# Kernel tuning notes

Measured on AMD Instinct MI355X. Metric: run time of the kernel, lower is better.

Reference implementation:

```python
import jax, jax.numpy as jnp
import numpy as np

B, T, H = 32, 64, 1024  # batch_size, input_number, hidden_size


def _lstm_cell(x, h, c, Wih, Whh, bih, bhh):
    # torch.nn.LSTMCell math: gate order i, f, g, o
    gates = x @ Wih.T + bih + h @ Whh.T + bhh
    i, f, g, o = jnp.split(gates, 4, axis=-1)
    c = jax.nn.sigmoid(f) * c + jax.nn.sigmoid(i) * jnp.tanh(g)
    h = jax.nn.sigmoid(o) * jnp.tanh(c)
    return h, c


def setup_inputs() -> dict:
    key = jax.random.key(0)
    ks = iter(jax.random.split(key, 64))

    def unif(shape, fan):
        s = 1.0 / np.sqrt(fan)
        return jax.random.uniform(next(ks), shape, jnp.float32, -s, s)

    inp = {
        'apperances': jax.random.normal(next(ks), (B, T, 2 * H), jnp.float32),
        'motions': jax.random.normal(next(ks), (B, T, 2 * H), jnp.float32),
    }
    # four LSTM cells: 1a/1m take 2H input, 2a/2m take H input
    for name, in_dim in [('1a', 2 * H), ('2a', H), ('1m', 2 * H), ('2m', H)]:
        inp['Wih_' + name] = unif((4 * H, in_dim), H)
        inp['Whh_' + name] = unif((4 * H, H), H)
        inp['bih_' + name] = unif((4 * H,), H)
        inp['bhh_' + name] = unif((4 * H,), H)
    # two-stream memory fusion (stand-in for MemoryRamTwoStreamModule)
    inp['Wg'] = unif((H, 2 * H), 2 * H)
    inp['bg'] = unif((H,), 2 * H)
    inp['Wa'] = unif((H, H), H)
    inp['ba'] = unif((H,), H)
    inp['Wm'] = unif((H, H), H)
    inp['bm'] = unif((H,), H)
    return inp


def reference(apperances, motions,
              Wih_1a, Whh_1a, bih_1a, bhh_1a,
              Wih_2a, Whh_2a, bih_2a, bhh_2a,
              Wih_1m, Whh_1m, bih_1m, bhh_1m,
              Wih_2m, Whh_2m, bih_2m, bhh_2m,
              Wg, bg, Wa, ba, Wm, bm):
    b, t, _ = apperances.shape
    h = Whh_1a.shape[1]
    xa = jnp.swapaxes(apperances, 0, 1)  # (T, B, 2H)
    xm = jnp.swapaxes(motions, 0, 1)     # (T, B, 2H)
    z = jnp.zeros((b, h), apperances.dtype)

    def step(carry, xs):
        h1a, c1a, h2a, c2a, h1m, c1m, h2m, c2m = carry
        xa_t, xm_t = xs
        h1m, c1m = _lstm_cell(xm_t, h1m, c1m, Wih_1m, Whh_1m, bih_1m, bhh_1m)
        h2m, c2m = _lstm_cell(h1m, h2m, c2m, Wih_2m, Whh_2m, bih_2m, bhh_2m)
        h1a, c1a = _lstm_cell(xa_t, h1a, c1a, Wih_1a, Whh_1a, bih_1a, bhh_1a)
        h2a, c2a = _lstm_cell(h1a, h2a, c2a, Wih_2a, Whh_2a, bih_2a, bhh_2a)
        return (h1a, c1a, h2a, c2a, h1m, c1m, h2m, c2m), (h2a, h2m)

    _, (Ha, Hm) = jax.lax.scan(step, (z, z, z, z, z, z, z, z), (xa, xm))
    Ha = jnp.swapaxes(Ha, 0, 1)  # (B, T, H)
    Hm = jnp.swapaxes(Hm, 0, 1)  # (B, T, H)
    # gated two-stream fusion per timestep (assumed MemoryRamTwoStreamModule)
    g = jax.nn.sigmoid(jnp.einsum('btk,hk->bth', jnp.concatenate([Ha, Hm], -1), Wg) + bg)
    mem = g * jnp.tanh(Ha @ Wa.T + ba) + (1.0 - g) * jnp.tanh(Hm @ Wm.T + bm)
    return mem  # (B, T, H)
```

## Files before the change

kernel.cpp:

```cpp
#include <hip/hip_runtime.h>
#include <cstdint>

typedef _Float16 f16;
typedef _Float16 f16x4v __attribute__((ext_vector_type(4)));
typedef _Float16 f16x8 __attribute__((ext_vector_type(8)));
typedef float f32x4 __attribute__((ext_vector_type(4)));

#define DEV static __device__ __forceinline__

#define GLDS16(gp, lp) __builtin_amdgcn_global_load_lds( \
    (const __attribute__((address_space(1))) void*)(gp), \
    (__attribute__((address_space(3))) void*)(lp), 16, 0, 0)

DEV float sigf(float x) { return 1.0f / (1.0f + __expf(-x)); }
DEV float tanh2(float x) {
  float e = __expf(-2.0f * fabsf(x));
  float t = (1.0f - e) / (1.0f + e);
  return x >= 0.0f ? t : -t;
}

DEV void waitflags(const unsigned* fp, int l) {
  unsigned f;
  do {
    f = __hip_atomic_load(fp + l, __ATOMIC_RELAXED, __HIP_MEMORY_SCOPE_AGENT);
  } while (__any(f == 0));
  asm volatile("" ::: "memory");
  __builtin_amdgcn_sched_barrier(0);
}

__global__ __launch_bounds__(256) void k_cvt(const float* __restrict__ s,
                                             f16* __restrict__ d, int n) {
  int i = (blockIdx.x * 256 + threadIdx.x) * 4;
  if (i >= n) return;
  float4 v = *(const float4*)(s + i);
  f16x4v o;
  o.x = (f16)v.x; o.y = (f16)v.y; o.z = (f16)v.z; o.w = (f16)v.w;
  *(f16x4v*)(d + i) = o;
}

__global__ __launch_bounds__(256) void k_packw1(const float* __restrict__ W,
                                                f16* __restrict__ P) {
  int i2 = blockIdx.x * 256 + threadIdx.x;
  int l = i2 & 63, frag = i2 >> 6;
  int kt = frag & 31, ug = frag >> 5;
  int gate = ug & 3, ut = ug >> 2;
  int row = gate * 1024 + ut * 16 + (l & 15);
  int k = kt * 32 + 8 * (l >> 4);
  const float* s = W + row * 1024 + k;
  f16x8 o;
#pragma unroll
  for (int j = 0; j < 8; ++j) o[j] = (f16)s[j];
  *(f16x8*)(P + frag * 512 + l * 8) = o;
}

__global__ __launch_bounds__(256) void k_packw2(const float* __restrict__ Wih,
                                                const float* __restrict__ Whh,
                                                f16* __restrict__ P) {
  int i2 = blockIdx.x * 256 + threadIdx.x;
  int l = i2 & 63, frag = i2 >> 6;
  int kt = frag & 63, ug = frag >> 6;
  int gate = ug & 3, ut = ug >> 2;
  int row = gate * 1024 + ut * 16 + (l & 15);
  int k = kt * 32 + 8 * (l >> 4);
  const float* s = (k < 1024) ? (Wih + row * 1024 + k)
                              : (Whh + row * 1024 + (k - 1024));
  f16x8 o;
#pragma unroll
  for (int j = 0; j < 8; ++j) o[j] = (f16)s[j];
  *(f16x8*)(P + frag * 512 + l * 8) = o;
}

template <int NKT, int LDA>
__global__ __launch_bounds__(256) void k_igemm(
    const f16* __restrict__ A0, const f16* __restrict__ A1,
    const f16* __restrict__ B0, const f16* __restrict__ B1,
    const float* __restrict__ bi0, const float* __restrict__ bh0,
    const float* __restrict__ bi1, const float* __restrict__ bh1,
    f16* __restrict__ C0, f16* __restrict__ C1) {
  const f16* A = blockIdx.z ? A1 : A0;
  const f16* B = blockIdx.z ? B1 : B0;
  const float* bi = blockIdx.z ? bi1 : bi0;
  const float* bh = blockIdx.z ? bh1 : bh0;
  f16* C = blockIdx.z ? C1 : C0;

  __shared__ alignas(16) f16 As[128 * 64];
  __shared__ alignas(16) f16 Bs[128 * 64];

  int tid = threadIdx.x, l = tid & 63, w = tid >> 6;
  int m0 = blockIdx.x * 128, n0 = blockIdx.y * 128;
  int wm = (w & 1) * 64, wn = (w >> 1) * 64;
  int lr = l & 15, lg = l >> 4;
  int sr = w * 32 + (l >> 3);
  int sc = (l & 7) * 8;

  f32x4 acc[4][4];
  f32x4 zero = {0.f, 0.f, 0.f, 0.f};
#pragma unroll
  for (int mt = 0; mt < 4; ++mt)
#pragma unroll
    for (int nt = 0; nt < 4; ++nt) acc[mt][nt] = zero;

  for (int kt = 0; kt < NKT; ++kt) {
    int k0 = kt * 64;
#pragma unroll
    for (int c2 = 0; c2 < 4; ++c2) {
      GLDS16(A + (size_t)(m0 + sr + c2 * 8) * LDA + k0 + sc, &As[(w * 32 + c2 * 8) * 64]);
      GLDS16(B + (size_t)(n0 + sr + c2 * 8) * LDA + k0 + sc, &Bs[(w * 32 + c2 * 8) * 64]);
    }
    __syncthreads();
#pragma unroll
    for (int ks = 0; ks < 2; ++ks) {
      f16x8 af[4], bf[4];
#pragma unroll
      for (int mt = 0; mt < 4; ++mt)
        af[mt] = *(const f16x8*)&As[(wm + mt * 16 + lr) * 64 + ks * 32 + 8 * lg];
#pragma unroll
      for (int nt = 0; nt < 4; ++nt)
        bf[nt] = *(const f16x8*)&Bs[(wn + nt * 16 + lr) * 64 + ks * 32 + 8 * lg];
#pragma unroll
      for (int mt = 0; mt < 4; ++mt)
#pragma unroll
        for (int nt = 0; nt < 4; ++nt)
          acc[mt][nt] = __builtin_amdgcn_mfma_f32_16x16x32_f16(af[mt], bf[nt], acc[mt][nt], 0, 0, 0);
    }
    __syncthreads();
  }

#pragma unroll
  for (int nt = 0; nt < 4; ++nt) {
    int n = n0 + wn + nt * 16 + lr;
    float bsum = bi[n] + bh[n];
#pragma unroll
    for (int mt = 0; mt < 4; ++mt) {
      int m = m0 + wm + mt * 16 + lg * 4;
#pragma unroll
      for (int r = 0; r < 4; ++r)
        C[(size_t)(m + r) * 4096 + n] = (f16)(acc[mt][nt][r] + bsum);
    }
  }
}

__global__ __launch_bounds__(512, 1) void k_scan2(
    const f16* __restrict__ Wp1_a, const f16* __restrict__ Wp1_m,
    const f16* __restrict__ Wp2_a, const f16* __restrict__ Wp2_m,
    const f16* __restrict__ G_a, const f16* __restrict__ G_m,
    const float* __restrict__ bi2_a, const float* __restrict__ bh2_a,
    const float* __restrict__ bi2_m, const float* __restrict__ bh2_m,
    f16* __restrict__ H1h,
    f16* __restrict__ h2c,
    f16* __restrict__ HaHm,
    unsigned* __restrict__ flags1,
    unsigned* __restrict__ flags2) {
  int bi = blockIdx.x;
  int role = bi >> 7, s = (bi >> 6) & 1, ut = bi & 63, u0 = ut * 16;
  int tid = threadIdx.x, l = tid & 63, w = tid >> 6;
  int lr = l & 15, lg = l >> 4;
  const f16* G = s ? G_m : G_a;
  f16* H1s = H1h + (size_t)s * 64 * 32768;
  f16* h2s = h2c + (size_t)s * 64 * 32768;
  f16* H2o = HaHm + s * 1024;

  f16x8 wreg[8][4];
  if (role == 0) {
    const f16* Wp = s ? Wp1_m : Wp1_a;
#pragma unroll
    for (int ks = 0; ks < 4; ++ks)
#pragma unroll
      for (int g = 0; g < 4; ++g) {
        wreg[ks][g] = *(const f16x8*)(Wp + (size_t)((ut * 4 + g) * 32 + (w * 4 + ks)) * 512 + l * 8);
        asm volatile("" : "+v"(wreg[ks][g]));
      }
  } else {
    const f16* Wp = s ? Wp2_m : Wp2_a;
#pragma unroll
    for (int ks = 0; ks < 8; ++ks)
#pragma unroll
      for (int g = 0; g < 4; ++g) {
        wreg[ks][g] = *(const f16x8*)(Wp + (size_t)((ut * 4 + g) * 64 + (w * 8 + ks)) * 512 + l * 8);
        asm volatile("" : "+v"(wreg[ks][g]));
      }
  }

  __shared__ alignas(16) float red[8][64][33];
  __shared__ alignas(16) f16 Gs[32][4][16];

  int eb = tid >> 4, eu = tid & 15;
  int emt = eb >> 4, elg = (eb >> 2) & 3, er = eb & 3;
  int lred = elg * 16 + eu;
  int idxb = emt * 16 + er;
  float creg = 0.f;
  f32x4 zero = {0.f, 0.f, 0.f, 0.f};

  if (role == 0) {
    int pb = tid >> 4, pg2 = (tid >> 2) & 3, p4 = tid & 3;
    int cb = w * 128;
    for (int t = 0; t < 64; ++t) {
      f16x4v gfrag = *(const f16x4v*)(G + (size_t)(pb * 64 + t) * 4096 + pg2 * 1024 + u0 + p4 * 4);

      f32x4 acc[2][4];
#pragma unroll
      for (int mt = 0; mt < 2; ++mt)
#pragma unroll
        for (int g = 0; g < 4; ++g) acc[mt][g] = zero;

      if (t > 0) {
        if (w == 0) waitflags(flags1 + (size_t)(s * 64 + t - 1) * 64, l);
        __syncthreads();
        const f16* hp = H1s + (size_t)(t - 1) * 32768;
        f16x8 A0[4], A1[4];
#pragma unroll
        for (int ks = 0; ks < 4; ++ks) {
          int col = cb + ks * 32 + 8 * lg;
          A0[ks] = *(const f16x8*)(hp + lr * 1024 + col);
          A1[ks] = *(const f16x8*)(hp + (16 + lr) * 1024 + col);
        }
#pragma unroll
        for (int ks = 0; ks < 4; ++ks)
#pragma unroll
          for (int g = 0; g < 4; ++g) {
            acc[0][g] = __builtin_amdgcn_mfma_f32_16x16x32_f16(A0[ks], wreg[ks][g], acc[0][g], 0, 0, 0);
            acc[1][g] = __builtin_amdgcn_mfma_f32_16x16x32_f16(A1[ks], wreg[ks][g], acc[1][g], 0, 0, 0);
          }
      }

      *(f16x4v*)&Gs[pb][pg2][p4 * 4] = gfrag;
#pragma unroll
      for (int mt = 0; mt < 2; ++mt)
#pragma unroll
        for (int g = 0; g < 4; ++g)
#pragma unroll
          for (int r = 0; r < 4; ++r)
            red[w][l][(mt * 4 + g) * 4 + r] = acc[mt][g][r];
      __syncthreads();

      float pre[4];
#pragma unroll
      for (int g = 0; g < 4; ++g) {
        int idx = idxb + g * 4;
        pre[g] = red[0][lred][idx] + red[1][lred][idx] + red[2][lred][idx] +
                 red[3][lred][idx] + red[4][lred][idx] + red[5][lred][idx] +
                 red[6][lred][idx] + red[7][lred][idx] + (float)Gs[eb][g][eu];
      }
      float cn = sigf(pre[1]) * creg + sigf(pre[0]) * tanh2(pre[2]);
      creg = cn;
      union { unsigned short us; f16 h; } cv;
      cv.h = (f16)(sigf(pre[3]) * tanh2(cn));
      unsigned ov = (unsigned)__shfl_xor((int)(unsigned)cv.us, 1, 64);
      if (!(tid & 1)) {
        unsigned pkv = ((unsigned)cv.us) | (ov << 16);
        __hip_atomic_store((unsigned*)(H1s + (size_t)t * 32768 + eb * 1024 + u0 + eu), pkv,
                           __ATOMIC_RELAXED, __HIP_MEMORY_SCOPE_AGENT);
      }
      asm volatile("s_waitcnt vmcnt(0)" ::: "memory");
      __syncthreads();
      if (tid == 0)
        __hip_atomic_store(flags1 + (size_t)(s * 64 + t) * 64 + ut, 1u,
                           __ATOMIC_RELAXED, __HIP_MEMORY_SCOPE_AGENT);
    }
  } else {
    const float* bip = s ? bi2_m : bi2_a;
    const float* bhp = s ? bh2_m : bh2_a;
    float b2r[4];
#pragma unroll
    for (int g = 0; g < 4; ++g)
      b2r[g] = bip[g * 1024 + u0 + eu] + bhp[g * 1024 + u0 + eu];
    int cb = (w & 3) * 256;

    for (int t = 0; t < 64; ++t) {
      f32x4 acc[2][4];
#pragma unroll
      for (int mt = 0; mt < 2; ++mt)
#pragma unroll
        for (int g = 0; g < 4; ++g) acc[mt][g] = zero;

      if (w == 0) waitflags(flags1 + (size_t)(s * 64 + t) * 64, l);
      if (t > 0 && w == 4) waitflags(flags2 + (size_t)(s * 64 + t - 1) * 64, l);
      __syncthreads();

      if (w < 4) {
        const f16* hp = H1s + (size_t)t * 32768;
        f16x8 A0[4], A1[4], B0[4], B1[4];
#pragma unroll
        for (int ks = 0; ks < 4; ++ks) {
          int c0 = cb + ks * 32 + 8 * lg;
          int c1 = cb + (4 + ks) * 32 + 8 * lg;
          A0[ks] = *(const f16x8*)(hp + lr * 1024 + c0);
          A1[ks] = *(const f16x8*)(hp + (16 + lr) * 1024 + c0);
          B0[ks] = *(const f16x8*)(hp + lr * 1024 + c1);
          B1[ks] = *(const f16x8*)(hp + (16 + lr) * 1024 + c1);
        }
#pragma unroll
        for (int ks = 0; ks < 4; ++ks)
#pragma unroll
          for (int g = 0; g < 4; ++g) {
            acc[0][g] = __builtin_amdgcn_mfma_f32_16x16x32_f16(A0[ks], wreg[ks][g], acc[0][g], 0, 0, 0);
            acc[1][g] = __builtin_amdgcn_mfma_f32_16x16x32_f16(A1[ks], wreg[ks][g], acc[1][g], 0, 0, 0);
          }
#pragma unroll
        for (int ks = 0; ks < 4; ++ks)
#pragma unroll
          for (int g = 0; g < 4; ++g) {
            acc[0][g] = __builtin_amdgcn_mfma_f32_16x16x32_f16(B0[ks], wreg[4 + ks][g], acc[0][g], 0, 0, 0);
            acc[1][g] = __builtin_amdgcn_mfma_f32_16x16x32_f16(B1[ks], wreg[4 + ks][g], acc[1][g], 0, 0, 0);
          }
      } else if (t > 0) {
        const f16* hp = h2s + (size_t)(t - 1) * 32768;
        f16x8 A0[4], A1[4], B0[4], B1[4];
#pragma unroll
        for (int ks = 0; ks < 4; ++ks) {
          int c0 = cb + ks * 32 + 8 * lg;
          int c1 = cb + (4 + ks) * 32 + 8 * lg;
          A0[ks] = *(const f16x8*)(hp + lr * 1024 + c0);
          A1[ks] = *(const f16x8*)(hp + (16 + lr) * 1024 + c0);
          B0[ks] = *(const f16x8*)(hp + lr * 1024 + c1);
          B1[ks] = *(const f16x8*)(hp + (16 + lr) * 1024 + c1);
        }
#pragma unroll
        for (int ks = 0; ks < 4; ++ks)
#pragma unroll
          for (int g = 0; g < 4; ++g) {
            acc[0][g] = __builtin_amdgcn_mfma_f32_16x16x32_f16(A0[ks], wreg[ks][g], acc[0][g], 0, 0, 0);
            acc[1][g] = __builtin_amdgcn_mfma_f32_16x16x32_f16(A1[ks], wreg[ks][g], acc[1][g], 0, 0, 0);
          }
#pragma unroll
        for (int ks = 0; ks < 4; ++ks)
#pragma unroll
          for (int g = 0; g < 4; ++g) {
            acc[0][g] = __builtin_amdgcn_mfma_f32_16x16x32_f16(B0[ks], wreg[4 + ks][g], acc[0][g], 0, 0, 0);
            acc[1][g] = __builtin_amdgcn_mfma_f32_16x16x32_f16(B1[ks], wreg[4 + ks][g], acc[1][g], 0, 0, 0);
          }
      }

#pragma unroll
      for (int mt = 0; mt < 2; ++mt)
#pragma unroll
        for (int g = 0; g < 4; ++g)
#pragma unroll
          for (int r = 0; r < 4; ++r)
            red[w][l][(mt * 4 + g) * 4 + r] = acc[mt][g][r];
      __syncthreads();

      float pre[4];
#pragma unroll
      for (int g = 0; g < 4; ++g) {
        int idx = idxb + g * 4;
        pre[g] = red[0][lred][idx] + red[1][lred][idx] + red[2][lred][idx] +
                 red[3][lred][idx] + red[4][lred][idx] + red[5][lred][idx] +
                 red[6][lred][idx] + red[7][lred][idx] + b2r[g];
      }
      float cn = sigf(pre[1]) * creg + sigf(pre[0]) * tanh2(pre[2]);
      creg = cn;
      union { unsigned short us; f16 h; } cv;
      cv.h = (f16)(sigf(pre[3]) * tanh2(cn));
      unsigned ov = (unsigned)__shfl_xor((int)(unsigned)cv.us, 1, 64);
      if (!(tid & 1)) {
        unsigned pkv = ((unsigned)cv.us) | (ov << 16);
        __hip_atomic_store((unsigned*)(h2s + (size_t)t * 32768 + eb * 1024 + u0 + eu), pkv,
                           __ATOMIC_RELAXED, __HIP_MEMORY_SCOPE_AGENT);
        *(unsigned*)(H2o + (size_t)(eb * 64 + t) * 2048 + u0 + eu) = pkv;
      }
      asm volatile("s_waitcnt vmcnt(0)" ::: "memory");
      __syncthreads();
      if (tid == 0)
        __hip_atomic_store(flags2 + (size_t)(s * 64 + t) * 64 + ut, 1u,
                           __ATOMIC_RELAXED, __HIP_MEMORY_SCOPE_AGENT);
    }
  }
}

DEV void gemm_phase(const f16* __restrict__ H, int kA0,
                    const f16* __restrict__ Bp, int brs, int nk,
                    f16* As, f16* Bs, int m0, int n0, int w, int l,
                    int wm, int wn, f32x4 (&acc)[4][2]) {
  f32x4 zero = {0.f, 0.f, 0.f, 0.f};
#pragma unroll
  for (int mt = 0; mt < 4; ++mt)
#pragma unroll
    for (int nt = 0; nt < 2; ++nt) acc[mt][nt] = zero;
  int lr = l & 15, lg = l >> 4;
  int sc = (l & 7) * 8;
  for (int kt = 0; kt < nk; ++kt) {
    int ka = kA0 + kt * 64, kb = kt * 64;
#pragma unroll
    for (int c2 = 0; c2 < 4; ++c2)
      GLDS16(H + (size_t)(m0 + w * 32 + c2 * 8 + (l >> 3)) * 2048 + ka + sc,
             As + (w * 32 + c2 * 8) * 64);
#pragma unroll
    for (int c2 = 0; c2 < 2; ++c2)
      GLDS16(Bp + (size_t)(n0 + w * 16 + c2 * 8 + (l >> 3)) * brs + kb + sc,
             Bs + (w * 16 + c2 * 8) * 64);
    __syncthreads();
#pragma unroll
    for (int ks = 0; ks < 2; ++ks) {
      f16x8 af[4], bf[2];
#pragma unroll
      for (int mt = 0; mt < 4; ++mt)
        af[mt] = *(const f16x8*)&As[(wm + mt * 16 + lr) * 64 + ks * 32 + 8 * lg];
#pragma unroll
      for (int nt = 0; nt < 2; ++nt)
        bf[nt] = *(const f16x8*)&Bs[(wn + nt * 16 + lr) * 64 + ks * 32 + 8 * lg];
#pragma unroll
      for (int mt = 0; mt < 4; ++mt)
#pragma unroll
        for (int nt = 0; nt < 2; ++nt)
          acc[mt][nt] = __builtin_amdgcn_mfma_f32_16x16x32_f16(af[mt], bf[nt], acc[mt][nt], 0, 0, 0);
    }
    __syncthreads();
  }
}

__global__ __launch_bounds__(256) void k_fusion(
    const f16* __restrict__ H, const f16* __restrict__ Wg16,
    const f16* __restrict__ Wa16, const f16* __restrict__ Wm16,
    const float* __restrict__ bg, const float* __restrict__ ba,
    const float* __restrict__ bm, float* __restrict__ out) {
  __shared__ alignas(16) f16 As[128 * 64];
  __shared__ alignas(16) f16 Bs[64 * 64];
  int tid = threadIdx.x, l = tid & 63, w = tid >> 6;
  int m0 = blockIdx.x * 128, n0 = blockIdx.y * 64;
  int wm = (w & 1) * 64, wn = (w >> 1) * 32;
  int lr = l & 15, lg = l >> 4;

  f32x4 acc[4][2];
  float ta[4][2][4], tm[4][2][4];

  gemm_phase(H, 0, Wa16, 1024, 16, As, Bs, m0, n0, w, l, wm, wn, acc);
#pragma unroll
  for (int nt = 0; nt < 2; ++nt) {
    float bv = ba[n0 + wn + nt * 16 + lr];
#pragma unroll
    for (int mt = 0; mt < 4; ++mt)
#pragma unroll
      for (int r = 0; r < 4; ++r) ta[mt][nt][r] = tanh2(acc[mt][nt][r] + bv);
  }
  gemm_phase(H, 1024, Wm16, 1024, 16, As, Bs, m0, n0, w, l, wm, wn, acc);
#pragma unroll
  for (int nt = 0; nt < 2; ++nt) {
    float bv = bm[n0 + wn + nt * 16 + lr];
#pragma unroll
    for (int mt = 0; mt < 4; ++mt)
#pragma unroll
      for (int r = 0; r < 4; ++r) tm[mt][nt][r] = tanh2(acc[mt][nt][r] + bv);
  }
  gemm_phase(H, 0, Wg16, 2048, 32, As, Bs, m0, n0, w, l, wm, wn, acc);
#pragma unroll
  for (int nt = 0; nt < 2; ++nt) {
    int n = n0 + wn + nt * 16 + lr;
    float bv = bg[n];
#pragma unroll
    for (int mt = 0; mt < 4; ++mt) {
      int m = m0 + wm + mt * 16 + lg * 4;
#pragma unroll
      for (int r = 0; r < 4; ++r) {
        float g = sigf(acc[mt][nt][r] + bv);
        out[(size_t)(m + r) * 1024 + n] = tm[mt][nt][r] + g * (ta[mt][nt][r] - tm[mt][nt][r]);
      }
    }
  }
}

extern "C" void kernel_launch(void* const* d_in, const int* in_sizes, int n_in,
                              void* d_out, int out_size, void* d_ws, size_t ws_size,
                              hipStream_t stream) {
  const float* xa = (const float*)d_in[0];
  const float* xm = (const float*)d_in[1];
  const float* Wih_1a = (const float*)d_in[2];
  const float* Whh_1a = (const float*)d_in[3];
  const float* bih_1a = (const float*)d_in[4];
  const float* bhh_1a = (const float*)d_in[5];
  const float* Wih_2a = (const float*)d_in[6];
  const float* Whh_2a = (const float*)d_in[7];
  const float* bih_2a = (const float*)d_in[8];
  const float* bhh_2a = (const float*)d_in[9];
  const float* Wih_1m = (const float*)d_in[10];
  const float* Whh_1m = (const float*)d_in[11];
  const float* bih_1m = (const float*)d_in[12];
  const float* bhh_1m = (const float*)d_in[13];
  const float* Wih_2m = (const float*)d_in[14];
  const float* Whh_2m = (const float*)d_in[15];
  const float* bih_2m = (const float*)d_in[16];
  const float* bhh_2m = (const float*)d_in[17];
  const float* Wg = (const float*)d_in[18];
  const float* bg = (const float*)d_in[19];
  const float* Wa = (const float*)d_in[20];
  const float* ba = (const float*)d_in[21];
  const float* Wm = (const float*)d_in[22];
  const float* bm = (const float*)d_in[23];

  char* ws = (char*)d_ws;
  const size_t MB = 1024ull * 1024;
  if (ws_size < 138 * MB) return;

  f16* x16a    = (f16*)(ws + 0 * MB);
  f16* x16m    = (f16*)(ws + 8 * MB);
  f16* W1ih16a = (f16*)(ws + 16 * MB);
  f16* W1ih16m = (f16*)(ws + 32 * MB);
  f16* W1p_a   = (f16*)(ws + 48 * MB);
  f16* W1p_m   = (f16*)(ws + 56 * MB);
  f16* W2p_a   = (f16*)(ws + 64 * MB);
  f16* W2p_m   = (f16*)(ws + 80 * MB);
  f16* Wg16    = (f16*)(ws + 96 * MB);
  f16* Wa16    = (f16*)(ws + 100 * MB);
  f16* Wm16    = (f16*)(ws + 102 * MB);
  f16* G0a     = (f16*)(ws + 104 * MB);
  f16* G0m     = (f16*)(ws + 120 * MB);
  unsigned* flags1 = (unsigned*)(ws + 136 * MB);
  unsigned* flags2 = (unsigned*)(ws + 136 * MB + 32768);
  f16* HaHm    = (f16*)(ws + 0 * MB);
  f16* H1h     = (f16*)(ws + 8 * MB);
  f16* h2c     = (f16*)(ws + 16 * MB);

  dim3 B256(256);
  k_cvt<<<4096, B256, 0, stream>>>(xa, x16a, 4194304);
  k_cvt<<<4096, B256, 0, stream>>>(xm, x16m, 4194304);
  k_cvt<<<8192, B256, 0, stream>>>(Wih_1a, W1ih16a, 8388608);
  k_cvt<<<8192, B256, 0, stream>>>(Wih_1m, W1ih16m, 8388608);
  k_cvt<<<2048, B256, 0, stream>>>(Wg, Wg16, 2097152);
  k_cvt<<<1024, B256, 0, stream>>>(Wa, Wa16, 1048576);
  k_cvt<<<1024, B256, 0, stream>>>(Wm, Wm16, 1048576);
  k_packw1<<<2048, B256, 0, stream>>>(Whh_1a, W1p_a);
  k_packw1<<<2048, B256, 0, stream>>>(Whh_1m, W1p_m);
  k_packw2<<<4096, B256, 0, stream>>>(Wih_2a, Whh_2a, W2p_a);
  k_packw2<<<4096, B256, 0, stream>>>(Wih_2m, Whh_2m, W2p_m);
  hipMemsetAsync(flags1, 0, 65536, stream);

  k_igemm<32, 2048><<<dim3(16, 32, 2), B256, 0, stream>>>(
      x16a, x16m, W1ih16a, W1ih16m, bih_1a, bhh_1a, bih_1m, bhh_1m, G0a, G0m);

  k_scan2<<<256, dim3(512), 0, stream>>>(
      W1p_a, W1p_m, W2p_a, W2p_m, G0a, G0m,
      bih_2a, bhh_2a, bih_2m, bhh_2m, H1h, h2c, HaHm, flags1, flags2);

  k_fusion<<<dim3(16, 16), B256, 0, stream>>>(HaHm, Wg16, Wa16, Wm16, bg, ba,
                                              bm, (float*)d_out);
}
```

Measured before the change: 755.4 us.

## Replace block barriers in scan with per-wave flag polling and LDS double buffering

The recurrent scan kernel stops using block-wide barriers around flag waits. Each wave now polls only the producer flags for the slice of H it reads, and publishes its step through a shared-memory counter so the last finishing wave sets the global flag. The reduction buffers are double-buffered by timestep parity so the trailing barrier can be removed, and the eleven preprocessing launches are merged into three kernels. This cuts barrier stalls and launch overhead on the latency-bound serial recurrence, but it adds twice the LDS for the reduction buffers and more intricate memory-ordering reasoning.

```diff
diff --git a/kernel.cpp b/kernel.cpp
--- a/kernel.cpp
+++ b/kernel.cpp
@@ -19,27 +19,36 @@
   return x >= 0.0f ? t : -t;
 }
 
-DEV void waitflags(const unsigned* fp, int l) {
-  unsigned f;
-  do {
-    f = __hip_atomic_load(fp + l, __ATOMIC_RELAXED, __HIP_MEMORY_SCOPE_AGENT);
-  } while (__any(f == 0));
-  asm volatile("" ::: "memory");
-  __builtin_amdgcn_sched_barrier(0);
-}
-
-__global__ __launch_bounds__(256) void k_cvt(const float* __restrict__ s,
-                                             f16* __restrict__ d, int n) {
-  int i = (blockIdx.x * 256 + threadIdx.x) * 4;
-  if (i >= n) return;
+__global__ __launch_bounds__(256) void k_cvt_all(
+    const float* __restrict__ s0, f16* __restrict__ d0,
+    const float* __restrict__ s1, f16* __restrict__ d1,
+    const float* __restrict__ s2, f16* __restrict__ d2,
+    const float* __restrict__ s3, f16* __restrict__ d3,
+    const float* __restrict__ s4, f16* __restrict__ d4,
+    const float* __restrict__ s5, f16* __restrict__ d5,
+    const float* __restrict__ s6, f16* __restrict__ d6) {
+  int bid = blockIdx.x;
+  const float* s; f16* d; int base;
+  if (bid < 4096)       { s = s0; d = d0; base = bid; }
+  else if (bid < 8192)  { s = s1; d = d1; base = bid - 4096; }
+  else if (bid < 16384) { s = s2; d = d2; base = bid - 8192; }
+  else if (bid < 24576) { s = s3; d = d3; base = bid - 16384; }
+  else if (bid < 26624) { s = s4; d = d4; base = bid - 24576; }
+  else if (bid < 27648) { s = s5; d = d5; base = bid - 26624; }
+  else                  { s = s6; d = d6; base = bid - 27648; }
+  int i = (base * 256 + threadIdx.x) * 4;
   float4 v = *(const float4*)(s + i);
   f16x4v o;
   o.x = (f16)v.x; o.y = (f16)v.y; o.z = (f16)v.z; o.w = (f16)v.w;
   *(f16x4v*)(d + i) = o;
 }
 
-__global__ __launch_bounds__(256) void k_packw1(const float* __restrict__ W,
-                                                f16* __restrict__ P) {
+__global__ __launch_bounds__(256) void k_packw1(const float* __restrict__ Wa,
+                                                const float* __restrict__ Wm,
+                                                f16* __restrict__ Pa,
+                                                f16* __restrict__ Pm) {
+  const float* W = blockIdx.y ? Wm : Wa;
+  f16* P = blockIdx.y ? Pm : Pa;
   int i2 = blockIdx.x * 256 + threadIdx.x;
   int l = i2 & 63, frag = i2 >> 6;
   int kt = frag & 31, ug = frag >> 5;
@@ -53,9 +62,15 @@
   *(f16x8*)(P + frag * 512 + l * 8) = o;
 }
 
-__global__ __launch_bounds__(256) void k_packw2(const float* __restrict__ Wih,
-                                                const float* __restrict__ Whh,
-                                                f16* __restrict__ P) {
+__global__ __launch_bounds__(256) void k_packw2(const float* __restrict__ Wiha,
+                                                const float* __restrict__ Whha,
+                                                const float* __restrict__ Wihm,
+                                                const float* __restrict__ Whhm,
+                                                f16* __restrict__ Pa,
+                                                f16* __restrict__ Pm) {
+  const float* Wih = blockIdx.y ? Wihm : Wiha;
+  const float* Whh = blockIdx.y ? Whhm : Whha;
+  f16* P = blockIdx.y ? Pm : Pa;
   int i2 = blockIdx.x * 256 + threadIdx.x;
   int l = i2 & 63, frag = i2 >> 6;
   int kt = frag & 63, ug = frag >> 6;
@@ -181,8 +196,11 @@
       }
   }
 
-  __shared__ alignas(16) float red[8][64][33];
-  __shared__ alignas(16) f16 Gs[32][4][16];
+  __shared__ alignas(16) float red[2][8][64][33];
+  __shared__ alignas(16) f16 Gs[2][32][4][16];
+  __shared__ unsigned wdone[64];
+  if (tid < 64) wdone[tid] = 0;
+  __syncthreads();
 
   int eb = tid >> 4, eu = tid & 15;
   int emt = eb >> 4, elg = (eb >> 2) & 3, er = eb & 3;
@@ -195,6 +213,7 @@
     int pb = tid >> 4, pg2 = (tid >> 2) & 3, p4 = tid & 3;
     int cb = w * 128;
     for (int t = 0; t < 64; ++t) {
+      int pp = t & 1;
       f16x4v gfrag = *(const f16x4v*)(G + (size_t)(pb * 64 + t) * 4096 + pg2 * 1024 + u0 + p4 * 4);
 
       f32x4 acc[2][4];
@@ -204,8 +223,14 @@
         for (int g = 0; g < 4; ++g) acc[mt][g] = zero;
 
       if (t > 0) {
-        if (w == 0) waitflags(flags1 + (size_t)(s * 64 + t - 1) * 64, l);
-        __syncthreads();
+        const unsigned* fp = flags1 + (size_t)(s * 64 + t - 1) * 64 + 8 * w;
+        unsigned f;
+        do {
+          f = (l < 8) ? __hip_atomic_load(fp + l, __ATOMIC_RELAXED,
+                                          __HIP_MEMORY_SCOPE_AGENT) : 1u;
+        } while (__any(f == 0));
+        asm volatile("" ::: "memory");
+        __builtin_amdgcn_sched_barrier(0);
         const f16* hp = H1s + (size_t)(t - 1) * 32768;
         f16x8 A0[4], A1[4];
 #pragma unroll
@@ -223,23 +248,25 @@
           }
       }
 
-      *(f16x4v*)&Gs[pb][pg2][p4 * 4] = gfrag;
+      *(f16x4v*)&Gs[pp][pb][pg2][p4 * 4] = gfrag;
 #pragma unroll
       for (int mt = 0; mt < 2; ++mt)
 #pragma unroll
         for (int g = 0; g < 4; ++g)
 #pragma unroll
           for (int r = 0; r < 4; ++r)
-            red[w][l][(mt * 4 + g) * 4 + r] = acc[mt][g][r];
+            red[pp][w][l][(mt * 4 + g) * 4 + r] = acc[mt][g][r];
       __syncthreads();
 
       float pre[4];
 #pragma unroll
       for (int g = 0; g < 4; ++g) {
         int idx = idxb + g * 4;
-        pre[g] = red[0][lred][idx] + red[1][lred][idx] + red[2][lred][idx] +
-                 red[3][lred][idx] + red[4][lred][idx] + red[5][lred][idx] +
-                 red[6][lred][idx] + red[7][lred][idx] + (float)Gs[eb][g][eu];
+        pre[g] = red[pp][0][lred][idx] + red[pp][1][lred][idx] +
+                 red[pp][2][lred][idx] + red[pp][3][lred][idx] +
+                 red[pp][4][lred][idx] + red[pp][5][lred][idx] +
+                 red[pp][6][lred][idx] + red[pp][7][lred][idx] +
+                 (float)Gs[pp][eb][g][eu];
       }
       float cn = sigf(pre[1]) * creg + sigf(pre[0]) * tanh2(pre[2]);
       creg = cn;
@@ -252,10 +279,15 @@
                            __ATOMIC_RELAXED, __HIP_MEMORY_SCOPE_AGENT);
       }
       asm volatile("s_waitcnt vmcnt(0)" ::: "memory");
-      __syncthreads();
-      if (tid == 0)
-        __hip_atomic_store(flags1 + (size_t)(s * 64 + t) * 64 + ut, 1u,
-                           __ATOMIC_RELAXED, __HIP_MEMORY_SCOPE_AGENT);
+      if (l == 0) {
+        unsigned ret = __hip_atomic_fetch_add(&wdone[t], 1u, __ATOMIC_RELAXED,
+                                              __HIP_MEMORY_SCOPE_WORKGROUP);
+        if (ret == 7u) {
+          asm volatile("" ::: "memory");
+          __hip_atomic_store(flags1 + (size_t)(s * 64 + t) * 64 + ut, 1u,
+                             __ATOMIC_RELAXED, __HIP_MEMORY_SCOPE_AGENT);
+        }
+      }
     }
   } else {
     const float* bip = s ? bi2_m : bi2_a;
@@ -267,17 +299,22 @@
     int cb = (w & 3) * 256;
 
     for (int t = 0; t < 64; ++t) {
+      int pp = t & 1;
       f32x4 acc[2][4];
 #pragma unroll
       for (int mt = 0; mt < 2; ++mt)
 #pragma unroll
         for (int g = 0; g < 4; ++g) acc[mt][g] = zero;
 
-      if (w == 0) waitflags(flags1 + (size_t)(s * 64 + t) * 64, l);
-      if (t > 0 && w == 4) waitflags(flags2 + (size_t)(s * 64 + t - 1) * 64, l);
-      __syncthreads();
-
       if (w < 4) {
+        const unsigned* fp = flags1 + (size_t)(s * 64 + t) * 64 + 16 * (w & 3);
+        unsigned f;
+        do {
+          f = (l < 16) ? __hip_atomic_load(fp + l, __ATOMIC_RELAXED,
+                                           __HIP_MEMORY_SCOPE_AGENT) : 1u;
+        } while (__any(f == 0));
+        asm volatile("" ::: "memory");
+        __builtin_amdgcn_sched_barrier(0);
         const f16* hp = H1s + (size_t)t * 32768;
         f16x8 A0[4], A1[4], B0[4], B1[4];
 #pragma unroll
@@ -304,6 +341,14 @@
             acc[1][g] = __builtin_amdgcn_mfma_f32_16x16x32_f16(B1[ks], wreg[4 + ks][g], acc[1][g], 0, 0, 0);
           }
       } else if (t > 0) {
+        const unsigned* fp = flags2 + (size_t)(s * 64 + t - 1) * 64 + 16 * (w & 3);
+        unsigned f;
+        do {
+          f = (l < 16) ? __hip_atomic_load(fp + l, __ATOMIC_RELAXED,
+                                           __HIP_MEMORY_SCOPE_AGENT) : 1u;
+        } while (__any(f == 0));
+        asm volatile("" ::: "memory");
+        __builtin_amdgcn_sched_barrier(0);
         const f16* hp = h2s + (size_t)(t - 1) * 32768;
         f16x8 A0[4], A1[4], B0[4], B1[4];
 #pragma unroll
@@ -337,16 +382,17 @@
         for (int g = 0; g < 4; ++g)
 #pragma unroll
           for (int r = 0; r < 4; ++r)
-            red[w][l][(mt * 4 + g) * 4 + r] = acc[mt][g][r];
+            red[pp][w][l][(mt * 4 + g) * 4 + r] = acc[mt][g][r];
       __syncthreads();
 
       float pre[4];
 #pragma unroll
       for (int g = 0; g < 4; ++g) {
         int idx = idxb + g * 4;
-        pre[g] = red[0][lred][idx] + red[1][lred][idx] + red[2][lred][idx] +
-                 red[3][lred][idx] + red[4][lred][idx] + red[5][lred][idx] +
-                 red[6][lred][idx] + red[7][lred][idx] + b2r[g];
+        pre[g] = red[pp][0][lred][idx] + red[pp][1][lred][idx] +
+                 red[pp][2][lred][idx] + red[pp][3][lred][idx] +
+                 red[pp][4][lred][idx] + red[pp][5][lred][idx] +
+                 red[pp][6][lred][idx] + red[pp][7][lred][idx] + b2r[g];
       }
       float cn = sigf(pre[1]) * creg + sigf(pre[0]) * tanh2(pre[2]);
       creg = cn;
@@ -360,10 +406,15 @@
         *(unsigned*)(H2o + (size_t)(eb * 64 + t) * 2048 + u0 + eu) = pkv;
       }
       asm volatile("s_waitcnt vmcnt(0)" ::: "memory");
-      __syncthreads();
-      if (tid == 0)
-        __hip_atomic_store(flags2 + (size_t)(s * 64 + t) * 64 + ut, 1u,
-                           __ATOMIC_RELAXED, __HIP_MEMORY_SCOPE_AGENT);
+      if (l == 0) {
+        unsigned ret = __hip_atomic_fetch_add(&wdone[t], 1u, __ATOMIC_RELAXED,
+                                              __HIP_MEMORY_SCOPE_WORKGROUP);
+        if (ret == 7u) {
+          asm volatile("" ::: "memory");
+          __hip_atomic_store(flags2 + (size_t)(s * 64 + t) * 64 + ut, 1u,
+                             __ATOMIC_RELAXED, __HIP_MEMORY_SCOPE_AGENT);
+        }
+      }
     }
   }
 }
@@ -511,17 +562,12 @@
   f16* h2c     = (f16*)(ws + 16 * MB);
 
   dim3 B256(256);
-  k_cvt<<<4096, B256, 0, stream>>>(xa, x16a, 4194304);
-  k_cvt<<<4096, B256, 0, stream>>>(xm, x16m, 4194304);
-  k_cvt<<<8192, B256, 0, stream>>>(Wih_1a, W1ih16a, 8388608);
-  k_cvt<<<8192, B256, 0, stream>>>(Wih_1m, W1ih16m, 8388608);
-  k_cvt<<<2048, B256, 0, stream>>>(Wg, Wg16, 2097152);
-  k_cvt<<<1024, B256, 0, stream>>>(Wa, Wa16, 1048576);
-  k_cvt<<<1024, B256, 0, stream>>>(Wm, Wm16, 1048576);
-  k_packw1<<<2048, B256, 0, stream>>>(Whh_1a, W1p_a);
-  k_packw1<<<2048, B256, 0, stream>>>(Whh_1m, W1p_m);
-  k_packw2<<<4096, B256, 0, stream>>>(Wih_2a, Whh_2a, W2p_a);
-  k_packw2<<<4096, B256, 0, stream>>>(Wih_2m, Whh_2m, W2p_m);
+  k_cvt_all<<<28672, B256, 0, stream>>>(xa, x16a, xm, x16m, Wih_1a, W1ih16a,
+                                        Wih_1m, W1ih16m, Wg, Wg16, Wa, Wa16,
+                                        Wm, Wm16);
+  k_packw1<<<dim3(2048, 2), B256, 0, stream>>>(Whh_1a, Whh_1m, W1p_a, W1p_m);
+  k_packw2<<<dim3(4096, 2), B256, 0, stream>>>(Wih_2a, Whh_2a, Wih_2m, Whh_2m,
+                                               W2p_a, W2p_m);
   hipMemsetAsync(flags1, 0, 65536, stream);
 
   k_igemm<32, 2048><<<dim3(16, 32, 2), B256, 0, stream>>>(
```

Result: slower. 826.4 us (+9.4%).
